# Kernel optimization log

Hardware: AMD Instinct MI355X
Metric: run time of the kernel (lower is better)

## Reference

```python
import jax, jax.numpy as jnp
import numpy as np
from jax import lax

B, C, N = 128, 320, 256
H = W = 16
GROUPS = 5
RATIO = 8
MASK_EPS = 1e-6   # registered buffer 'eps' in the torch module
GN_EPS = 1e-5     # torch GroupNorm default


def setup_inputs() -> dict:
    key = jax.random.key(0)
    ks = jax.random.split(key, 10)
    def rn(k, shape, scale=0.05):
        return jax.random.normal(k, shape, dtype=jnp.float32) * scale
    return {
        "x": jax.random.normal(ks[0], (B, C, N), dtype=jnp.float32),
        "low_cutoff": jnp.float32(0.2),
        "high_cutoff": jnp.float32(0.7),
        "ca_w1": rn(ks[1], (C // RATIO, C)),
        "ca_b1": jnp.zeros((C // RATIO,), jnp.float32),
        "ca_w2": rn(ks[2], (3 * C, C // RATIO)),
        "ca_b2": jnp.zeros((3 * C,), jnp.float32),
        "low_w": rn(ks[3], (C, C, 3, 3)),
        "low_b": jnp.zeros((C,), jnp.float32),
        "low_g": jnp.ones((C,), jnp.float32),
        "low_beta": jnp.zeros((C,), jnp.float32),
        "mid_w": rn(ks[4], (C, C, 3, 3)),
        "mid_b": jnp.zeros((C,), jnp.float32),
        "mid_g": jnp.ones((C,), jnp.float32),
        "mid_beta": jnp.zeros((C,), jnp.float32),
        "high_w": rn(ks[5], (C, C, 3, 3)),
        "high_b": jnp.zeros((C,), jnp.float32),
        "high_g": jnp.ones((C,), jnp.float32),
        "high_beta": jnp.zeros((C,), jnp.float32),
        "sa_w": rn(ks[6], (1, C, 1, 1)),
        "sa_b": jnp.zeros((1,), jnp.float32),
    }


def _conv3x3_gn(y, w, b, gamma, beta):
    # Conv2d(C,C,3,padding=1) -> GroupNorm(5,C)
    out = lax.conv_general_dilated(
        y, w, window_strides=(1, 1), padding='SAME',
        dimension_numbers=('NCHW', 'OIHW', 'NCHW'))
    out = out + b[None, :, None, None]
    b_, c_, h_, w_ = out.shape
    g = out.reshape(b_, GROUPS, c_ // GROUPS, h_, w_)
    mu = g.mean(axis=(2, 3, 4), keepdims=True)
    var = g.var(axis=(2, 3, 4), keepdims=True)
    g = (g - mu) * lax.rsqrt(var + GN_EPS)
    out = g.reshape(b_, c_, h_, w_)
    return out * gamma[None, :, None, None] + beta[None, :, None, None]


def reference(x, low_cutoff, high_cutoff, ca_w1, ca_b1, ca_w2, ca_b2,
              low_w, low_b, low_g, low_beta,
              mid_w, mid_b, mid_g, mid_beta,
              high_w, high_b, high_g, high_beta,
              sa_w, sa_b):
    b, c, n = x.shape
    n_pix = H * W
    # reshape_to_square (N == n_pix here, pad/slice kept for faithfulness)
    if n < n_pix:
        xp = jnp.pad(x, ((0, 0), (0, 0), (0, n_pix - n)))
    else:
        xp = x[:, :, :n_pix]
    x2d = xp.reshape(b, c, H, W)

    # DynamicFrequencyFilter: avgpool over N -> 1x1 conv1d -> relu -> 1x1 conv1d -> sigmoid
    avg = x.mean(axis=-1)                                  # [B, C]
    hcw = jax.nn.relu(avg @ ca_w1.T + ca_b1)               # [B, C//8]
    cw = jax.nn.sigmoid(hcw @ ca_w2.T + ca_b2)             # [B, 3C]
    cw = cw.reshape(b, 3, c, 1, 1)

    # FFT + shifted frequency masks. torch fftshift(dim=None) shifts all dims,
    # but the B/C shifts commute with the (B/C-broadcast) mask multiply and are
    # undone by ifftshift, so shifting only the spatial axes is equivalent.
    fft_feat = jnp.fft.fftshift(jnp.fft.fft2(x2d), axes=(-2, -1))
    yy, xx = jnp.meshgrid(jnp.linspace(-1.0, 1.0, H), jnp.linspace(-1.0, 1.0, W), indexing='ij')
    dist = jnp.sqrt(xx ** 2 + yy ** 2) / np.sqrt(2.0)
    low_mask = jax.nn.sigmoid((low_cutoff - dist) / MASK_EPS)
    mid_mask = jax.nn.sigmoid((dist - low_cutoff) / MASK_EPS) * jax.nn.sigmoid((high_cutoff - dist) / MASK_EPS)
    high_mask = jax.nn.sigmoid((dist - high_cutoff) / MASK_EPS)

    def band(mask):
        return jnp.fft.ifft2(jnp.fft.ifftshift(fft_feat * mask, axes=(-2, -1))).real

    low_feat = _conv3x3_gn(band(low_mask), low_w, low_b, low_g, low_beta) + x2d
    mid_feat = _conv3x3_gn(band(mid_mask), mid_w, mid_b, mid_g, mid_beta) + x2d
    high_feat = _conv3x3_gn(band(high_mask), high_w, high_b, high_g, high_beta) + x2d

    fused = cw[:, 0] * low_feat + cw[:, 1] * mid_feat + cw[:, 2] * high_feat

    # spatial attention: 1x1 conv C->1, sigmoid
    sw = jax.nn.sigmoid(jnp.einsum('bchw,c->bhw', fused, sa_w[0, :, 0, 0])[:, None] + sa_b[0])
    out = (fused * sw).reshape(b, c, n_pix)
    return out[:, :, :n]
```

## Files before the change

kernel.cpp:

```cpp
#include <hip/hip_runtime.h>
#include <math.h>

#define NB 128
#define NC 320
#define NG 5
#define CPG 64
#define NHID 40

typedef short bf16x8 __attribute__((ext_vector_type(8)));
typedef short s16x4  __attribute__((ext_vector_type(4)));
typedef float f32x4  __attribute__((ext_vector_type(4)));

__device__ __forceinline__ float sigf(float x){ return 1.0f/(1.0f+expf(-x)); }

__device__ __forceinline__ unsigned short f2b(float f){
  unsigned u = __float_as_uint(f);
  unsigned r = (u + 0x7fffu + ((u >> 16) & 1u)) >> 16;
  return (unsigned short)r;
}
__device__ __forceinline__ float b2f(unsigned short u){
  return __uint_as_float(((unsigned)u) << 16);
}

__device__ __forceinline__ void gll16(const void* g, void* l){
  __builtin_amdgcn_global_load_lds(
      (const __attribute__((address_space(1))) void*)g,
      (__attribute__((address_space(3))) void*)l, 16, 0, 0);
}

__global__ __launch_bounds__(256) void k_prep(const float* __restrict__ lowc,
                                              const float* __restrict__ highc,
                                              const float* __restrict__ w0,
                                              const float* __restrict__ w1,
                                              const float* __restrict__ w2,
                                              unsigned short* __restrict__ WgT,
                                              unsigned short* __restrict__ WAb){
  __shared__ float msh[256];
  __shared__ float cost[16];
  __shared__ float ksh[256];
  __shared__ float wsh[2880];
  int bid = blockIdx.x, t = threadIdx.x;

  if (bid < 768){
    int band = bid >> 8, p = bid & 255;
    float lc = lowc[0], hc = highc[0];
    {
      int a1 = t >> 4, a2 = t & 15;
      const float step = 2.0f / 15.0f;
      float cy = -1.0f + step * (float)a1;
      float cx = -1.0f + step * (float)a2;
      float dist = sqrtf(cx*cx + cy*cy) / 1.41421356237309515f;
      float m = band == 0 ? sigf((lc - dist) * 1e6f)
              : band == 1 ? sigf((dist - lc) * 1e6f) * sigf((hc - dist) * 1e6f)
                          : sigf((dist - hc) * 1e6f);
      msh[t] = m;
    }
    if (t < 16) cost[t] = cosf((float)t * 0.392699081698724154f);
    __syncthreads();
    {
      int d1 = t >> 4, d2 = t & 15;
      float s = 0.f;
      int ang0 = (8*d1 + 8*d2) & 15;
      for (int a1 = 0; a1 < 16; ++a1){
        int ang = (ang0 + a1*d1) & 15;
        #pragma unroll
        for (int a2 = 0; a2 < 16; ++a2){
          s += msh[a1*16 + a2] * cost[ang];
          ang = (ang + d2) & 15;
        }
      }
      ksh[t] = s * (1.0f/256.0f);
    }
    __syncthreads();
    int d1 = ((p >> 4) - (t >> 4)) & 15;
    int d2 = ((p & 15) - (t & 15)) & 15;
    WgT[(size_t)(band << 16) + (p << 8) + t] = f2b(ksh[(d1 << 4) | d2]);
  } else {
    int bid2 = bid - 768;
    int band = bid2 / 320, co = bid2 % 320;
    const float* w = band == 0 ? w0 : (band == 1 ? w1 : w2);
    const float* src = w + (size_t)co * 2880;
    for (int i = t; i < 2880; i += 256) wsh[i] = src[i];
    __syncthreads();
    unsigned short* dst = WAb + (size_t)band * 921600;
    for (int g = t; g < 360; g += 256){
      int tap = g / 40, r = g % 40;
      unsigned short tmp[8];
      #pragma unroll
      for (int j = 0; j < 8; ++j) tmp[j] = f2b(wsh[(r*8 + j)*9 + tap]);
      s16x4* o = (s16x4*)(dst + (size_t)g * 2560 + co*8);
      o[0] = *(s16x4*)tmp;
      o[1] = *(s16x4*)(tmp + 4);
    }
  }
}

__global__ __launch_bounds__(256, 4) void k_bandg3(const float* __restrict__ x,
                                                   const unsigned short* __restrict__ WgT,
                                                   unsigned short* __restrict__ bandT,
                                                   float* __restrict__ avgOut){
  __shared__ unsigned short xt[64*256];
  int tid = threadIdx.x;
  int wgid = (blockIdx.x & 7)*80 + (blockIdx.x >> 3);
  int b = wgid / 5, cq = wgid % 5;
  int cibase = cq * 64;
  size_t rowbase = (size_t)wgid * 64;

  {
    int r = tid >> 2, c0 = (tid & 3) * 64;
    const float* xp = x + (rowbase + r)*256 + c0;
    unsigned short* dp = xt + r*256;
    int sw = (r & 7) << 3;
    float rs = 0.f;
    #pragma unroll
    for (int j = 0; j < 64; j += 4){
      float4 f = *(const float4*)(xp + j);
      rs += f.x + f.y + f.z + f.w;
      unsigned short t4[4] = { f2b(f.x), f2b(f.y), f2b(f.z), f2b(f.w) };
      *(s16x4*)(dp + ((c0 + j) ^ sw)) = *(s16x4*)t4;
    }
    rs += __shfl_down(rs, 1);
    rs += __shfl_down(rs, 2);
    if ((tid & 3) == 0) avgOut[rowbase + r] = rs * (1.0f/256.0f);
  }

  for (int i = tid; i < 3264; i += 256){
    int band = i / 1088, r = i % 1088;
    int si = r >> 4, cg = r & 15;
    int rr, cc;
    if (si < 18)      { rr = 0;        cc = si;      }
    else if (si < 36) { rr = 17;       cc = si - 18; }
    else if (si < 52) { rr = si - 35;  cc = 0;       }
    else              { rr = si - 51;  cc = 17;      }
    s16x4 z = {0,0,0,0};
    *(s16x4*)(bandT + (size_t)band*13271040 +
              ((size_t)(b*324 + rr*18 + cc))*NC + cibase + cg*4) = z;
  }
  __syncthreads();

  int l  = tid & 63;
  int wq = tid >> 6;
  int cig = l >> 4, lan = l & 15;

  for (int band = 0; band < 3; ++band){
    const unsigned short* Wg = WgT + (size_t)band * 65536;
    unsigned short* bT = bandT + (size_t)band * 13271040;

    f32x4 acc[4][4];
    #pragma unroll
    for (int m = 0; m < 4; ++m)
      #pragma unroll
      for (int n = 0; n < 4; ++n) acc[m][n] = (f32x4){0.f,0.f,0.f,0.f};

    #pragma unroll 2
    for (int ks = 0; ks < 8; ++ks){
      int koff = ks*32 + cig*8;
      bf16x8 a[4], bv[4];
      #pragma unroll
      for (int m = 0; m < 4; ++m){
        int row = m*16 + lan;
        a[m] = *(const bf16x8*)(xt + row*256 + (koff ^ ((row & 7) << 3)));
      }
      #pragma unroll
      for (int n = 0; n < 4; ++n){
        int p = wq*64 + n*16 + lan;
        bv[n] = *(const bf16x8*)(Wg + (size_t)p*256 + koff);
      }
      #pragma unroll
      for (int m = 0; m < 4; ++m)
        #pragma unroll
        for (int n = 0; n < 4; ++n)
          acc[m][n] = __builtin_amdgcn_mfma_f32_16x16x32_bf16(a[m], bv[n], acc[m][n], 0, 0, 0);
    }

    #pragma unroll
    for (int m = 0; m < 4; ++m){
      #pragma unroll
      for (int n = 0; n < 4; ++n){
        int p = wq*64 + n*16 + lan;
        int slot = ((p >> 4) + 1) * 18 + (p & 15) + 1;
        int ci = cibase + m*16 + cig*4;
        unsigned short o[4] = { f2b(acc[m][n][0]), f2b(acc[m][n][1]),
                                f2b(acc[m][n][2]), f2b(acc[m][n][3]) };
        *(s16x4*)(bT + ((size_t)(b*324 + slot))*NC + ci) = *(s16x4*)o;
      }
    }
  }
}

__global__ __launch_bounds__(256, 2) void k_convg(const unsigned short* __restrict__ bandT,
                                                  const unsigned short* __restrict__ WAb,
                                                  const float* __restrict__ bias0,
                                                  const float* __restrict__ bias1,
                                                  const float* __restrict__ bias2,
                                                  unsigned short* __restrict__ convb,
                                                  float* __restrict__ stats_part){
  __shared__ char ldsB[2*11520];
  __shared__ float stw[4][5][2];

  int tid = threadIdx.x;
  int wgid = (blockIdx.x & 7)*192 + (blockIdx.x >> 3);
  int band = wgid / 512; int rem = wgid & 511;
  int b = rem >> 2, ch = (rem >> 1) & 1, ph = rem & 1;

  const unsigned short* bT = bandT + (size_t)band*13271040 + (size_t)b*103680;
  const unsigned short* WA = WAb + (size_t)band*921600;
  const float* bias = band == 0 ? bias0 : (band == 1 ? bias1 : bias2);
  unsigned short* cbp = convb + (size_t)band * 10485760;

  int l = tid & 63, w = tid >> 6;
  int wco = w >> 1, wpx = w & 1;
  int cig = l >> 4, lan = l & 15;
  int cobase = ch*160 + wco*80;
  int px0 = ph*128 + wpx*64;

  const unsigned short* Areg = WA + cig*2560 + ch*1280 + (wco*80 + lan)*8;

  int gb0 = tid, gb1 = tid + 256, gb2 = tid + 512;
  int boff0 = (ph*144 + gb0%180)*320 + (gb0/180)*8;
  int boff1 = (ph*144 + gb1%180)*320 + (gb1/180)*8;
  int boff2 = (ph*144 + gb2%180)*320 + (gb2/180)*8;

  int Bread0 = (cig*180 + (wpx*4 + 1)*18 + lan + 1)*16;

  f32x4 acc[5][4];
  #pragma unroll
  for (int m = 0; m < 5; ++m)
    #pragma unroll
    for (int n = 0; n < 4; ++n) acc[m][n] = (f32x4){0.f,0.f,0.f,0.f};

  bf16x8 A0[5], A1[5];

#define LOADA(ARR, OFS) do { \
    const unsigned short* p_ = Areg + (OFS); \
    ARR[0] = *(const bf16x8*)(p_); \
    ARR[1] = *(const bf16x8*)(p_ + 128); \
    ARR[2] = *(const bf16x8*)(p_ + 256); \
    ARR[3] = *(const bf16x8*)(p_ + 384); \
    ARR[4] = *(const bf16x8*)(p_ + 512); \
  } while(0)

#define STAGE_B(CN, BUF) do { \
    const unsigned short* sB = bT + (CN)*32; \
    char* dB = ldsB + (BUF)*11520; \
    gll16(sB + boff0, dB + tid*16); \
    gll16(sB + boff1, dB + 4096 + tid*16); \
    if (tid < 208) gll16(sB + boff2, dB + 8192 + tid*16); \
  } while(0)

  STAGE_B(0, 0);
  LOADA(A0, 0);
  asm volatile("s_waitcnt vmcnt(0)" ::: "memory");
  __builtin_amdgcn_s_barrier();

#define BODY(T, CURA, NXTA) do { \
    if ((T) == 0){ \
      __builtin_amdgcn_s_barrier(); \
      STAGE_B(cc2 + 1, 1); \
    } else if ((T) == 9){ \
      __builtin_amdgcn_s_barrier(); \
      if (cib2 < 4) STAGE_B(cc2 + 2, 0); \
    } \
    const char* Bb = ldsB + (((T) >= 9) ? 11520 : 0) + Bread0 \
                   + (((((T)%9)/3)*18 + (((T)%9)%3) - 19)*16); \
    bf16x8 b0 = *(const bf16x8*)(Bb); \
    bf16x8 b1 = *(const bf16x8*)(Bb + 288); \
    bf16x8 b2 = *(const bf16x8*)(Bb + 576); \
    bf16x8 b3 = *(const bf16x8*)(Bb + 864); \
    { \
      size_t ofs_ = ((T) == 17) ? (cc + 20480) \
          : ((size_t)(((((T)+1)%9))*102400) + cc + ((((T)+1) >= 9) ? 10240 : 0)); \
      LOADA(NXTA, ofs_); \
    } \
    __builtin_amdgcn_s_setprio(1); \
    acc[0][0]=__builtin_amdgcn_mfma_f32_16x16x32_bf16(CURA[0],b0,acc[0][0],0,0,0); \
    acc[0][1]=__builtin_amdgcn_mfma_f32_16x16x32_bf16(CURA[0],b1,acc[0][1],0,0,0); \
    acc[0][2]=__builtin_amdgcn_mfma_f32_16x16x32_bf16(CURA[0],b2,acc[0][2],0,0,0); \
    acc[0][3]=__builtin_amdgcn_mfma_f32_16x16x32_bf16(CURA[0],b3,acc[0][3],0,0,0); \
    acc[1][0]=__builtin_amdgcn_mfma_f32_16x16x32_bf16(CURA[1],b0,acc[1][0],0,0,0); \
    acc[1][1]=__builtin_amdgcn_mfma_f32_16x16x32_bf16(CURA[1],b1,acc[1][1],0,0,0); \
    acc[1][2]=__builtin_amdgcn_mfma_f32_16x16x32_bf16(CURA[1],b2,acc[1][2],0,0,0); \
    acc[1][3]=__builtin_amdgcn_mfma_f32_16x16x32_bf16(CURA[1],b3,acc[1][3],0,0,0); \
    acc[2][0]=__builtin_amdgcn_mfma_f32_16x16x32_bf16(CURA[2],b0,acc[2][0],0,0,0); \
    acc[2][1]=__builtin_amdgcn_mfma_f32_16x16x32_bf16(CURA[2],b1,acc[2][1],0,0,0); \
    acc[2][2]=__builtin_amdgcn_mfma_f32_16x16x32_bf16(CURA[2],b2,acc[2][2],0,0,0); \
    acc[2][3]=__builtin_amdgcn_mfma_f32_16x16x32_bf16(CURA[2],b3,acc[2][3],0,0,0); \
    acc[3][0]=__builtin_amdgcn_mfma_f32_16x16x32_bf16(CURA[3],b0,acc[3][0],0,0,0); \
    acc[3][1]=__builtin_amdgcn_mfma_f32_16x16x32_bf16(CURA[3],b1,acc[3][1],0,0,0); \
    acc[3][2]=__builtin_amdgcn_mfma_f32_16x16x32_bf16(CURA[3],b2,acc[3][2],0,0,0); \
    acc[3][3]=__builtin_amdgcn_mfma_f32_16x16x32_bf16(CURA[3],b3,acc[3][3],0,0,0); \
    acc[4][0]=__builtin_amdgcn_mfma_f32_16x16x32_bf16(CURA[4],b0,acc[4][0],0,0,0); \
    acc[4][1]=__builtin_amdgcn_mfma_f32_16x16x32_bf16(CURA[4],b1,acc[4][1],0,0,0); \
    acc[4][2]=__builtin_amdgcn_mfma_f32_16x16x32_bf16(CURA[4],b2,acc[4][2],0,0,0); \
    acc[4][3]=__builtin_amdgcn_mfma_f32_16x16x32_bf16(CURA[4],b3,acc[4][3],0,0,0); \
    __builtin_amdgcn_s_setprio(0); \
  } while(0)

  for (int cib2 = 0; cib2 < 5; ++cib2){
    int cc2 = cib2*2;
    size_t cc = (size_t)cib2 * 20480;
    BODY(0,  A0, A1);  BODY(1,  A1, A0);  BODY(2,  A0, A1);
    BODY(3,  A1, A0);  BODY(4,  A0, A1);  BODY(5,  A1, A0);
    BODY(6,  A0, A1);  BODY(7,  A1, A0);  BODY(8,  A0, A1);
    BODY(9,  A1, A0);  BODY(10, A0, A1);  BODY(11, A1, A0);
    BODY(12, A0, A1);  BODY(13, A1, A0);  BODY(14, A0, A1);
    BODY(15, A1, A0);  BODY(16, A0, A1);  BODY(17, A1, A0);
  }
#undef BODY
#undef STAGE_B
#undef LOADA

  #pragma unroll
  for (int m = 0; m < 5; ++m)
    #pragma unroll
    for (int r = 0; r < 4; ++r){
      float bvs = bias[cobase + m*16 + cig*4 + r];
      #pragma unroll
      for (int n = 0; n < 4; ++n) acc[m][n][r] += bvs;
    }

  #pragma unroll
  for (int m = 0; m < 5; ++m){
    float s = 0.f, q = 0.f;
    #pragma unroll
    for (int n = 0; n < 4; ++n)
      #pragma unroll
      for (int r = 0; r < 4; ++r){ float v = acc[m][n][r]; s += v; q += v*v; }
    #pragma unroll
    for (int o = 32; o > 0; o >>= 1){ s += __shfl_xor(s, o); q += __shfl_xor(q, o); }
    if (l == 0){ stw[w][m][0] = s; stw[w][m][1] = q; }
  }

  #pragma unroll
  for (int m = 0; m < 5; ++m)
    #pragma unroll
    for (int r = 0; r < 4; ++r){
      int co = cobase + m*16 + cig*4 + r;
      unsigned short* op = cbp + ((size_t)(b*NC + co))*256 + px0 + lan;
      #pragma unroll
      for (int n = 0; n < 4; ++n) op[n*16] = f2b(acc[m][n][r]);
    }

  __syncthreads();
  if (tid < 6){
    int gl = tid >> 1, comp = tid & 1;
    int g = ch*2 + gl;
    float t = 0.f;
    for (int w2 = 0; w2 < 4; ++w2)
      #pragma unroll
      for (int m = 0; m < 5; ++m)
        if (((ch*160 + (w2 >> 1)*80 + m*16) >> 6) == g) t += stw[w2][m][comp];
    stats_part[((size_t)(band*NB + b)*NG + g)*8 + ch*4 + ph*2 + comp] = t;
  }
}

__global__ __launch_bounds__(512) void k_fuse3(const unsigned short* __restrict__ cb0,
                                               const unsigned short* __restrict__ cb1,
                                               const unsigned short* __restrict__ cb2,
                                               const float* __restrict__ x,
                                               const float* __restrict__ stats_part,
                                               const float* __restrict__ g0, const float* __restrict__ be0,
                                               const float* __restrict__ g1, const float* __restrict__ be1,
                                               const float* __restrict__ g2, const float* __restrict__ be2,
                                               const float* __restrict__ avg,
                                               const float* __restrict__ caw1,
                                               const float* __restrict__ cab1,
                                               const float* __restrict__ caw2,
                                               const float* __restrict__ cab2,
                                               const float* __restrict__ saw,
                                               const float* __restrict__ sab,
                                               float* __restrict__ out){
  __shared__ unsigned short fl[NC*128];
  __shared__ float mu_s[3][NG], rs_s[3][NG], sh[4][128];
  __shared__ float avs[NC], hsh[NHID], cws[3*NC];
  int b = blockIdx.x >> 1, half = blockIdx.x & 1;
  int tid = threadIdx.x;

  if (tid < NC) avs[tid] = avg[b*NC + tid];
  else if (tid >= 496 && tid < 511){
    int t2 = tid - 496;
    int band = t2 / 5, g = t2 % 5;
    const float* sp = stats_part + ((size_t)(band*NB + b)*NG + g)*8;
    float s = 0.f, q = 0.f;
    if (g <= 2){ s += sp[0] + sp[2]; q += sp[1] + sp[3]; }
    if (g >= 2){ s += sp[4] + sp[6]; q += sp[5] + sp[7]; }
    float mu = s * (1.f/16384.f);
    float var = q * (1.f/16384.f) - mu*mu;
    mu_s[band][g] = mu; rs_s[band][g] = rsqrtf(var + 1e-5f);
  }
  __syncthreads();
  if (tid < NHID){
    float s = cab1[tid];
    const float* wr = caw1 + tid*NC;
    for (int i = 0; i < NC; ++i) s += wr[i] * avs[i];
    hsh[tid] = fmaxf(s, 0.0f);
  }
  __syncthreads();
  for (int o = tid; o < 3*NC; o += 512){
    float s = cab2[o];
    const float* wr = caw2 + o*NHID;
    #pragma unroll
    for (int i = 0; i < NHID; ++i) s += wr[i] * hsh[i];
    cws[o] = sigf(s);
  }
  __syncthreads();

  int p = tid & 127, cs = tid >> 7;
  int px = half*128 + p;
  float sacc = 0.f;
  for (int ci = cs; ci < NC; ci += 4){
    int g = ci >> 6;
    size_t idx = ((size_t)(b*NC + ci))*256 + px;
    float xv = x[idx];
    float f =
      cws[ci      ] * ((b2f(cb0[idx]) - mu_s[0][g])*rs_s[0][g]*g0[ci] + be0[ci] + xv) +
      cws[320 + ci] * ((b2f(cb1[idx]) - mu_s[1][g])*rs_s[1][g]*g1[ci] + be1[ci] + xv) +
      cws[640 + ci] * ((b2f(cb2[idx]) - mu_s[2][g])*rs_s[2][g]*g2[ci] + be2[ci] + xv);
    fl[ci*128 + p] = f2b(f);
    sacc += f * saw[ci];
  }
  sh[cs][p] = sacc;
  __syncthreads();
  if (tid < 128) sh[0][tid] = sigf(sh[0][tid] + sh[1][tid] + sh[2][tid] + sh[3][tid] + sab[0]);
  __syncthreads();
  float swv = sh[0][p];
  for (int ci = cs; ci < NC; ci += 4){
    size_t idx = ((size_t)(b*NC + ci))*256 + px;
    out[idx] = b2f(fl[ci*128 + p]) * swv;
  }
}

extern "C" void kernel_launch(void* const* d_in, const int* in_sizes, int n_in,
                              void* d_out, int out_size, void* d_ws, size_t ws_size,
                              hipStream_t stream){
  (void)in_sizes; (void)n_in; (void)out_size; (void)ws_size;
  const float* x     = (const float*)d_in[0];
  const float* lowc  = (const float*)d_in[1];
  const float* highc = (const float*)d_in[2];
  const float* ca_w1 = (const float*)d_in[3];
  const float* ca_b1 = (const float*)d_in[4];
  const float* ca_w2 = (const float*)d_in[5];
  const float* ca_b2 = (const float*)d_in[6];
  const float* conv_w[3] = {(const float*)d_in[7],  (const float*)d_in[11], (const float*)d_in[15]};
  const float* conv_b[3] = {(const float*)d_in[8],  (const float*)d_in[12], (const float*)d_in[16]};
  const float* gn_g[3]   = {(const float*)d_in[9],  (const float*)d_in[13], (const float*)d_in[17]};
  const float* gn_be[3]  = {(const float*)d_in[10], (const float*)d_in[14], (const float*)d_in[18]};
  const float* sa_w = (const float*)d_in[19];
  const float* sa_b = (const float*)d_in[20];
  float* out = (float*)d_out;

  char* base = (char*)d_ws;
  unsigned short* WgT   = (unsigned short*)(base + 4096);
  unsigned short* WAb   = (unsigned short*)(base + 397312);
  unsigned short* bandT = (unsigned short*)(base + 5926912);
  unsigned short* cbb   = (unsigned short*)(base + 85553152);
  float*          avg   = (float*)(base + 148959232);
  float*          stats = (float*)(base + 149123072);
  unsigned short* cb0 = cbb;
  unsigned short* cb1 = cbb + 10485760;
  unsigned short* cb2 = cbb + 20971520;

  k_prep  <<<1728, 256, 0, stream>>>(lowc, highc, conv_w[0], conv_w[1], conv_w[2],
                                     WgT, WAb);

  k_bandg3<<<640, 256, 0, stream>>>(x, WgT, bandT, avg);

  k_convg<<<1536, 256, 0, stream>>>(bandT, WAb, conv_b[0], conv_b[1], conv_b[2],
                                    cbb, stats);

  k_fuse3<<<256, 512, 0, stream>>>(cb0, cb1, cb2, x, stats,
                                   gn_g[0], gn_be[0], gn_g[1], gn_be[1], gn_g[2], gn_be[2],
                                   avg, ca_w1, ca_b1, ca_w2, ca_b2,
                                   sa_w, sa_b, out);
}
```

Baseline: 262.9 us.

## Split channel-attention MLP into own kernel and quarter fuse blocks per batch

Moves the channel-attention MLP, which k_fuse3 used to recompute redundantly in every block with mostly idle threads, into a separate small kernel that writes the per-batch weights to workspace. k_fuse3 now reads those weights from global memory and uses four blocks per batch over 64 pixels each instead of two over 128. The split removes duplicated serial MLP work and doubles the fuse grid for better occupancy and parallelism. In exchange it adds one kernel launch and a small global round-trip for the weights.

```diff
diff --git a/kernel.cpp b/kernel.cpp
--- a/kernel.cpp
+++ b/kernel.cpp
@@ -185,6 +185,31 @@
         *(s16x4*)(bT + ((size_t)(b*324 + slot))*NC + ci) = *(s16x4*)o;
       }
     }
+  }
+}
+
+__global__ __launch_bounds__(256) void k_ca(const float* __restrict__ avg,
+                                            const float* __restrict__ w1,
+                                            const float* __restrict__ b1,
+                                            const float* __restrict__ w2,
+                                            const float* __restrict__ b2,
+                                            float* __restrict__ cw){
+  __shared__ float a[NC];
+  __shared__ float h[NHID];
+  int b = blockIdx.x, t = threadIdx.x;
+  a[t] = avg[b * NC + t];
+  if (t < NC - 256) a[256 + t] = avg[b * NC + 256 + t];
+  __syncthreads();
+  if (t < NHID){
+    float s = b1[t];
+    for (int i = 0; i < NC; ++i) s += w1[t * NC + i] * a[i];
+    h[t] = fmaxf(s, 0.0f);
+  }
+  __syncthreads();
+  for (int o = t; o < 3 * NC; o += 256){
+    float s = b2[o];
+    for (int i = 0; i < NHID; ++i) s += w2[o * NHID + i] * h[i];
+    cw[b * (3 * NC) + o] = sigf(s);
   }
 }
 
@@ -362,24 +387,16 @@
                                                const float* __restrict__ g0, const float* __restrict__ be0,
                                                const float* __restrict__ g1, const float* __restrict__ be1,
                                                const float* __restrict__ g2, const float* __restrict__ be2,
-                                               const float* __restrict__ avg,
-                                               const float* __restrict__ caw1,
-                                               const float* __restrict__ cab1,
-                                               const float* __restrict__ caw2,
-                                               const float* __restrict__ cab2,
+                                               const float* __restrict__ cw,
                                                const float* __restrict__ saw,
                                                const float* __restrict__ sab,
                                                float* __restrict__ out){
-  __shared__ unsigned short fl[NC*128];
-  __shared__ float mu_s[3][NG], rs_s[3][NG], sh[4][128];
-  __shared__ float avs[NC], hsh[NHID], cws[3*NC];
-  int b = blockIdx.x >> 1, half = blockIdx.x & 1;
+  __shared__ unsigned short fl[NC*64];
+  __shared__ float mu_s[3][NG], rs_s[3][NG], sh[8][64];
+  int b = blockIdx.x >> 2, quarter = blockIdx.x & 3;
   int tid = threadIdx.x;
-
-  if (tid < NC) avs[tid] = avg[b*NC + tid];
-  else if (tid >= 496 && tid < 511){
-    int t2 = tid - 496;
-    int band = t2 / 5, g = t2 % 5;
+  if (tid < 15){
+    int band = tid / 5, g = tid % 5;
     const float* sp = stats_part + ((size_t)(band*NB + b)*NG + g)*8;
     float s = 0.f, q = 0.f;
     if (g <= 2){ s += sp[0] + sp[2]; q += sp[1] + sp[3]; }
@@ -389,44 +406,34 @@
     mu_s[band][g] = mu; rs_s[band][g] = rsqrtf(var + 1e-5f);
   }
   __syncthreads();
-  if (tid < NHID){
-    float s = cab1[tid];
-    const float* wr = caw1 + tid*NC;
-    for (int i = 0; i < NC; ++i) s += wr[i] * avs[i];
-    hsh[tid] = fmaxf(s, 0.0f);
-  }
-  __syncthreads();
-  for (int o = tid; o < 3*NC; o += 512){
-    float s = cab2[o];
-    const float* wr = caw2 + o*NHID;
-    #pragma unroll
-    for (int i = 0; i < NHID; ++i) s += wr[i] * hsh[i];
-    cws[o] = sigf(s);
-  }
-  __syncthreads();
-
-  int p = tid & 127, cs = tid >> 7;
-  int px = half*128 + p;
+
+  int p = tid & 63, cs = tid >> 6;
+  int px = quarter*64 + p;
   float sacc = 0.f;
-  for (int ci = cs; ci < NC; ci += 4){
+  const float* cwb = cw + b*960;
+  for (int ci = cs; ci < NC; ci += 8){
     int g = ci >> 6;
     size_t idx = ((size_t)(b*NC + ci))*256 + px;
     float xv = x[idx];
     float f =
-      cws[ci      ] * ((b2f(cb0[idx]) - mu_s[0][g])*rs_s[0][g]*g0[ci] + be0[ci] + xv) +
-      cws[320 + ci] * ((b2f(cb1[idx]) - mu_s[1][g])*rs_s[1][g]*g1[ci] + be1[ci] + xv) +
-      cws[640 + ci] * ((b2f(cb2[idx]) - mu_s[2][g])*rs_s[2][g]*g2[ci] + be2[ci] + xv);
-    fl[ci*128 + p] = f2b(f);
+      cwb[ci      ] * ((b2f(cb0[idx]) - mu_s[0][g])*rs_s[0][g]*g0[ci] + be0[ci] + xv) +
+      cwb[320 + ci] * ((b2f(cb1[idx]) - mu_s[1][g])*rs_s[1][g]*g1[ci] + be1[ci] + xv) +
+      cwb[640 + ci] * ((b2f(cb2[idx]) - mu_s[2][g])*rs_s[2][g]*g2[ci] + be2[ci] + xv);
+    fl[ci*64 + p] = f2b(f);
     sacc += f * saw[ci];
   }
   sh[cs][p] = sacc;
   __syncthreads();
-  if (tid < 128) sh[0][tid] = sigf(sh[0][tid] + sh[1][tid] + sh[2][tid] + sh[3][tid] + sab[0]);
+  if (tid < 64){
+    float s = sh[0][tid] + sh[1][tid] + sh[2][tid] + sh[3][tid]
+            + sh[4][tid] + sh[5][tid] + sh[6][tid] + sh[7][tid];
+    sh[0][tid] = sigf(s + sab[0]);
+  }
   __syncthreads();
   float swv = sh[0][p];
-  for (int ci = cs; ci < NC; ci += 4){
+  for (int ci = cs; ci < NC; ci += 8){
     size_t idx = ((size_t)(b*NC + ci))*256 + px;
-    out[idx] = b2f(fl[ci*128 + p]) * swv;
+    out[idx] = b2f(fl[ci*64 + p]) * swv;
   }
 }
 
@@ -456,6 +463,7 @@
   unsigned short* cbb   = (unsigned short*)(base + 85553152);
   float*          avg   = (float*)(base + 148959232);
   float*          stats = (float*)(base + 149123072);
+  float*          cw    = (float*)(base + 149184512);
   unsigned short* cb0 = cbb;
   unsigned short* cb1 = cbb + 10485760;
   unsigned short* cb2 = cbb + 20971520;
@@ -464,12 +472,12 @@
                                      WgT, WAb);
 
   k_bandg3<<<640, 256, 0, stream>>>(x, WgT, bandT, avg);
+  k_ca    <<<NB,  256, 0, stream>>>(avg, ca_w1, ca_b1, ca_w2, ca_b2, cw);
 
   k_convg<<<1536, 256, 0, stream>>>(bandT, WAb, conv_b[0], conv_b[1], conv_b[2],
                                     cbb, stats);
 
-  k_fuse3<<<256, 512, 0, stream>>>(cb0, cb1, cb2, x, stats,
+  k_fuse3<<<512, 512, 0, stream>>>(cb0, cb1, cb2, x, stats,
                                    gn_g[0], gn_be[0], gn_g[1], gn_be[1], gn_g[2], gn_be[2],
-                                   avg, ca_w1, ca_b1, ca_w2, ca_b2,
-                                   sa_w, sa_b, out);
-}
+                                   cw, sa_w, sa_b, out);
+}
```

New measurement: 255.5 us, median of 2. 1.03x faster.
